# Kernel tuning notes

Hardware: AMD Instinct MI355X
Metric: run time of the kernel (lower is better)

## Reference

```python
import jax, jax.numpy as jnp
import numpy as np

EMBED_DIM = 1024
NUM_HEADS = 16
HEAD_DIM = EMBED_DIM // NUM_HEADS
HIDDEN_DIM = int(EMBED_DIM * 4.0)
LN_EPS = 1e-5


def layer_norm(x, g, b):
    mu = jnp.mean(x, axis=-1, keepdims=True)
    var = jnp.var(x, axis=-1, keepdims=True)
    return (x - mu) * jax.lax.rsqrt(var + LN_EPS) * g + b


def setup_inputs() -> dict:
    key = jax.random.key(0)
    ks = jax.random.split(key, 8)
    D, H3, Dh = EMBED_DIM, 3 * EMBED_DIM, HIDDEN_DIM
    s = lambda fan: 1.0 / np.sqrt(fan)
    return {
        "x": jax.random.normal(ks[0], (2, 2048, D), dtype=jnp.float32),
        "ln1_g": jnp.ones((D,), jnp.float32),
        "ln1_b": jnp.zeros((D,), jnp.float32),
        "ln2_g": jnp.ones((D,), jnp.float32),
        "ln2_b": jnp.zeros((D,), jnp.float32),
        "w_qkv": jax.random.normal(ks[1], (D, H3), jnp.float32) * s(D),
        "b_qkv": jnp.zeros((H3,), jnp.float32),
        "w_proj": jax.random.normal(ks[2], (D, D), jnp.float32) * s(D),
        "b_proj": jnp.zeros((D,), jnp.float32),
        "w_fc1": jax.random.normal(ks[3], (D, Dh), jnp.float32) * s(D),
        "b_fc1": jnp.zeros((Dh,), jnp.float32),
        "w_fc2": jax.random.normal(ks[4], (Dh, D), jnp.float32) * s(Dh),
        "b_fc2": jnp.zeros((D,), jnp.float32),
    }


def reference(x, ln1_g, ln1_b, ln2_g, ln2_b, w_qkv, b_qkv, w_proj, b_proj,
              w_fc1, b_fc1, w_fc2, b_fc2):
    B, N, D = x.shape
    H, hd = NUM_HEADS, HEAD_DIM

    # --- attention branch (dropout inactive at eval) ---
    h = layer_norm(x, ln1_g, ln1_b)
    qkv = h @ w_qkv + b_qkv                      # [B,N,3D]
    qkv = qkv.reshape(B, N, 3, H, hd)
    q = qkv[:, :, 0].transpose(0, 2, 1, 3)       # [B,H,N,hd]
    k = qkv[:, :, 1].transpose(0, 2, 1, 3)
    v = qkv[:, :, 2].transpose(0, 2, 1, 3)
    scores = jnp.einsum('bhqd,bhkd->bhqk', q, k) / jnp.sqrt(jnp.float32(hd))
    attn = jax.nn.softmax(scores, axis=-1)
    ctx = jnp.einsum('bhqk,bhkd->bhqd', attn, v) # [B,H,N,hd]
    ctx = ctx.transpose(0, 2, 1, 3).reshape(B, N, D)
    x = x + ctx @ w_proj + b_proj

    # --- MLP branch ---
    h2 = layer_norm(x, ln2_g, ln2_b)
    h2 = jax.nn.gelu(h2 @ w_fc1 + b_fc1, approximate=False)  # torch nn.GELU = exact erf
    x = x + h2 @ w_fc2 + b_fc2
    return x
```

## Files before the change

### kernel.cpp

```cpp
#include <hip/hip_runtime.h>
#include <hip/hip_bf16.h>
#include <cstdint>

typedef __attribute__((ext_vector_type(8))) short short8;
typedef __attribute__((ext_vector_type(4))) float f32x4;

__device__ __forceinline__ uint16_t f2b(float f) {
  uint32_t u = __builtin_bit_cast(uint32_t, f);
  return (uint16_t)((u + 0x7FFFu + ((u >> 16) & 1u)) >> 16);
}
__device__ __forceinline__ float b2f(uint16_t h) {
  uint32_t u = ((uint32_t)h) << 16;
  return __builtin_bit_cast(float, u);
}
__device__ __forceinline__ void async16(void* lds, const void* g) {
  __builtin_amdgcn_global_load_lds(
      (const __attribute__((address_space(1))) uint32_t*)g,
      (__attribute__((address_space(3))) uint32_t*)lds, 16, 0, 0);
}
__device__ __forceinline__ void xcd_remap(int& bx, int& by, int& bz) {
  int gx = gridDim.x, gy = gridDim.y;
  int nwg = gx * gy * gridDim.z;
  int hw = blockIdx.x + gx * (blockIdx.y + gy * blockIdx.z);
  int work = ((nwg & 7) == 0) ? ((hw & 7) * (nwg >> 3) + (hw >> 3)) : hw;
  bx = work % gx;
  int t = work / gx;
  by = t % gy;
  bz = t / gy;
}

__global__ __launch_bounds__(256) void k_transpose_all(
    const float* __restrict__ wq, const float* __restrict__ wp,
    const float* __restrict__ w1, const float* __restrict__ w2,
    uint16_t* __restrict__ tq, uint16_t* __restrict__ tp,
    uint16_t* __restrict__ t1, uint16_t* __restrict__ t2) {
  __shared__ float tile[64][65];
  int id = blockIdx.x;
  const float* w; uint16_t* wT; int K, N, bx, by;
  if (id < 768)        { w = wq; wT = tq; K = 1024; N = 3072; bx = id % 48; by = id / 48; }
  else if (id < 1024)  { id -= 768;  w = wp; wT = tp; K = 1024; N = 1024; bx = id & 15; by = id >> 4; }
  else if (id < 2048)  { id -= 1024; w = w1; wT = t1; K = 1024; N = 4096; bx = id & 63; by = id >> 6; }
  else                 { id -= 2048; w = w2; wT = t2; K = 4096; N = 1024; bx = id & 15; by = id >> 4; }
  const int tx = threadIdx.x;
  const int k0 = by * 64, n0 = bx * 64;
  const int cr = tx & 15, rbase = tx >> 4;
#pragma unroll
  for (int rr = 0; rr < 4; ++rr) {
    int k = rbase + rr * 16;
    int n = cr * 4;
    float4 v = *(const float4*)&w[(size_t)(k0 + k) * N + (n0 + n)];
    tile[k][n + 0] = v.x; tile[k][n + 1] = v.y;
    tile[k][n + 2] = v.z; tile[k][n + 3] = v.w;
  }
  __syncthreads();
#pragma unroll
  for (int rr = 0; rr < 4; ++rr) {
    int n = rbase + rr * 16;
    int k = cr * 4;
    ushort4 o;
    o.x = f2b(tile[k + 0][n]);
    o.y = f2b(tile[k + 1][n]);
    o.z = f2b(tile[k + 2][n]);
    o.w = f2b(tile[k + 3][n]);
    *(ushort4*)&wT[(size_t)(n0 + n) * K + (k0 + k)] = o;
  }
}

__global__ __launch_bounds__(256) void k_layernorm(
    const float* __restrict__ x, const float* __restrict__ g,
    const float* __restrict__ b, uint16_t* __restrict__ out) {
  const int row = blockIdx.x * 4 + (threadIdx.x >> 6);
  const int lane = threadIdx.x & 63;
  const float* xr = x + (size_t)row * 1024;
  float4 v[4];
  float s = 0.f, ss = 0.f;
#pragma unroll
  for (int i = 0; i < 4; ++i) {
    v[i] = *(const float4*)&xr[i * 256 + lane * 4];
    s += v[i].x + v[i].y + v[i].z + v[i].w;
    ss += v[i].x * v[i].x + v[i].y * v[i].y + v[i].z * v[i].z + v[i].w * v[i].w;
  }
#pragma unroll
  for (int off = 1; off < 64; off <<= 1) {
    s += __shfl_xor(s, off);
    ss += __shfl_xor(ss, off);
  }
  float mu = s * (1.f / 1024.f);
  float rstd = rsqrtf(ss * (1.f / 1024.f) - mu * mu + 1e-5f);
#pragma unroll
  for (int i = 0; i < 4; ++i) {
    int col = i * 256 + lane * 4;
    float4 gv = *(const float4*)&g[col];
    float4 bv = *(const float4*)&b[col];
    ushort4 o;
    o.x = f2b((v[i].x - mu) * rstd * gv.x + bv.x);
    o.y = f2b((v[i].y - mu) * rstd * gv.y + bv.y);
    o.z = f2b((v[i].z - mu) * rstd * gv.z + bv.z);
    o.w = f2b((v[i].w - mu) * rstd * gv.w + bv.w);
    *(ushort4*)&out[(size_t)row * 1024 + col] = o;
  }
}

__global__ __launch_bounds__(256) void k_ln2_fuse(
    const float* __restrict__ x, const uint16_t* __restrict__ pp0,
    const uint16_t* __restrict__ pp1, const float* __restrict__ bias,
    const float* __restrict__ g, const float* __restrict__ b,
    float* __restrict__ x2, uint16_t* __restrict__ out) {
  const int row = blockIdx.x * 4 + (threadIdx.x >> 6);
  const int lane = threadIdx.x & 63;
  const size_t rb = (size_t)row * 1024;
  float4 v[4];
  float s = 0.f, ss = 0.f;
#pragma unroll
  for (int i = 0; i < 4; ++i) {
    int col = i * 256 + lane * 4;
    float4 xv = *(const float4*)&x[rb + col];
    float4 bv = *(const float4*)&bias[col];
    ushort4 a0 = *(const ushort4*)&pp0[rb + col];
    ushort4 a1 = *(const ushort4*)&pp1[rb + col];
    v[i].x = xv.x + bv.x + b2f(a0.x) + b2f(a1.x);
    v[i].y = xv.y + bv.y + b2f(a0.y) + b2f(a1.y);
    v[i].z = xv.z + bv.z + b2f(a0.z) + b2f(a1.z);
    v[i].w = xv.w + bv.w + b2f(a0.w) + b2f(a1.w);
    *(float4*)&x2[rb + col] = v[i];
    s += v[i].x + v[i].y + v[i].z + v[i].w;
    ss += v[i].x * v[i].x + v[i].y * v[i].y + v[i].z * v[i].z + v[i].w * v[i].w;
  }
#pragma unroll
  for (int off = 1; off < 64; off <<= 1) {
    s += __shfl_xor(s, off);
    ss += __shfl_xor(ss, off);
  }
  float mu = s * (1.f / 1024.f);
  float rstd = rsqrtf(ss * (1.f / 1024.f) - mu * mu + 1e-5f);
#pragma unroll
  for (int i = 0; i < 4; ++i) {
    int col = i * 256 + lane * 4;
    float4 gv = *(const float4*)&g[col];
    float4 bv = *(const float4*)&b[col];
    ushort4 o;
    o.x = f2b((v[i].x - mu) * rstd * gv.x + bv.x);
    o.y = f2b((v[i].y - mu) * rstd * gv.y + bv.y);
    o.z = f2b((v[i].z - mu) * rstd * gv.z + bv.z);
    o.w = f2b((v[i].w - mu) * rstd * gv.w + bv.w);
    *(ushort4*)&out[rb + col] = o;
  }
}

__global__ __launch_bounds__(256) void k_fc2_reduce(
    const float* __restrict__ x2, const uint16_t* __restrict__ f0,
    const uint16_t* __restrict__ f1, const uint16_t* __restrict__ f2,
    const uint16_t* __restrict__ f3, const float* __restrict__ bias,
    float* __restrict__ out, int N) {
  int i = (blockIdx.x * 256 + threadIdx.x) * 4;
  float4 v = *(const float4*)&x2[i];
  float4 bv = *(const float4*)&bias[i & (N - 1)];
  ushort4 a0 = *(const ushort4*)&f0[i];
  ushort4 a1 = *(const ushort4*)&f1[i];
  ushort4 a2 = *(const ushort4*)&f2[i];
  ushort4 a3 = *(const ushort4*)&f3[i];
  v.x += bv.x + b2f(a0.x) + b2f(a1.x) + b2f(a2.x) + b2f(a3.x);
  v.y += bv.y + b2f(a0.y) + b2f(a1.y) + b2f(a2.y) + b2f(a3.y);
  v.z += bv.z + b2f(a0.z) + b2f(a1.z) + b2f(a2.z) + b2f(a3.z);
  v.w += bv.w + b2f(a0.w) + b2f(a1.w) + b2f(a2.w) + b2f(a3.w);
  *(float4*)&out[i] = v;
}

template <int EPI>
__global__ __launch_bounds__(256) void k_gemm(
    const uint16_t* __restrict__ A, const uint16_t* __restrict__ Bt,
    const float* __restrict__ bias, void* __restrict__ Cout,
    uint16_t* __restrict__ vTout, int M, int N, int K) {
  __shared__ __align__(16) uint16_t Alds[128 * 64];
  __shared__ __align__(16) uint16_t Blds[128 * 64];
  int bx, by, bz;
  xcd_remap(bx, by, bz);
  const int tid = threadIdx.x;
  const int lane = tid & 63;
  const int w = tid >> 6;
  const int wr = w >> 1, wc = w & 1;
  const int m0 = by * 128, n0 = bx * 128;
  const int l15 = lane & 15, l4 = lane >> 4;
  f32x4 acc[4][4] = {};
  for (int k0 = 0; k0 < K; k0 += 64) {
#pragma unroll
    for (int c = 0; c < 4; ++c) {
      int i = c * 256 + tid;
      int row = i >> 3, d = (i & 7) * 8;
      async16(&Alds[i * 8], &A[(size_t)(m0 + row) * K + k0 + d]);
    }
#pragma unroll
    for (int c = 0; c < 4; ++c) {
      int i = c * 256 + tid;
      int row = i >> 3, d = (i & 7) * 8;
      async16(&Blds[i * 8], &Bt[(size_t)(n0 + row) * K + k0 + d]);
    }
    __syncthreads();
#pragma unroll
    for (int kc = 0; kc < 2; ++kc) {
      short8 af[4], bf[4];
#pragma unroll
      for (int m = 0; m < 4; ++m)
        af[m] = *(const short8*)&Alds[(wr * 64 + m * 16 + l15) * 64 + kc * 32 + l4 * 8];
#pragma unroll
      for (int n = 0; n < 4; ++n)
        bf[n] = *(const short8*)&Blds[(wc * 64 + n * 16 + l15) * 64 + kc * 32 + l4 * 8];
#pragma unroll
      for (int m = 0; m < 4; ++m)
#pragma unroll
        for (int n = 0; n < 4; ++n)
          acc[m][n] = __builtin_amdgcn_mfma_f32_16x16x32_bf16(af[m], bf[n], acc[m][n], 0, 0, 0);
    }
    __syncthreads();
  }
#pragma unroll
  for (int m = 0; m < 4; ++m) {
#pragma unroll
    for (int n = 0; n < 4; ++n) {
      int col = n0 + wc * 64 + n * 16 + l15;
      int rowb = m0 + wr * 64 + m * 16 + l4 * 4;
      float bv = bias[col];
      if constexpr (EPI == 3) {
        if (col >= 2048) {
          int dtot = col - 2048;
          int hh = dtot >> 6, dd = dtot & 63;
          int bg = rowb >> 11, tl = rowb & 2047;
          ushort4 ov;
          ov.x = f2b(acc[m][n][0] + bv);
          ov.y = f2b(acc[m][n][1] + bv);
          ov.z = f2b(acc[m][n][2] + bv);
          ov.w = f2b(acc[m][n][3] + bv);
          *(ushort4*)&vTout[(((size_t)(bg * 16 + hh)) * 64 + dd) * 2048 + tl] = ov;
          continue;
        }
      }
#pragma unroll
      for (int r = 0; r < 4; ++r) {
        float val = acc[m][n][r] + bv;
        size_t idx = (size_t)(rowb + r) * N + col;
        if constexpr (EPI == 2) {
          float u = val * val;
          float a = fmaf(u, 0.1029480545f, 2.3022078158f);
          float t = exp2f(val * a);
          float gl = val - val / (t + 1.0f);
          ((uint16_t*)Cout)[idx] = f2b(gl);
        } else {
          ((uint16_t*)Cout)[idx] = f2b(val);
        }
      }
    }
  }
}

__global__ __launch_bounds__(256) void k_gemm_splitk(
    const uint16_t* __restrict__ A, const uint16_t* __restrict__ Bt,
    uint16_t* __restrict__ p0, uint16_t* __restrict__ p1,
    uint16_t* __restrict__ p2, uint16_t* __restrict__ p3,
    int M, int N, int K, int Kc) {
  __shared__ __align__(16) uint16_t Alds[128 * 64];
  __shared__ __align__(16) uint16_t Blds[128 * 64];
  int bx, by, bz;
  xcd_remap(bx, by, bz);
  const int tid = threadIdx.x;
  const int lane = tid & 63;
  const int w = tid >> 6;
  const int wr = w >> 1, wc = w & 1;
  const int m0 = by * 128, n0 = bx * 128;
  const int l15 = lane & 15, l4 = lane >> 4;
  const int kbeg = bz * Kc, kend = kbeg + Kc;
  uint16_t* __restrict__ P = (bz == 0) ? p0 : (bz == 1) ? p1 : (bz == 2) ? p2 : p3;
  f32x4 acc[4][4] = {};
  for (int k0 = kbeg; k0 < kend; k0 += 64) {
#pragma unroll
    for (int c = 0; c < 4; ++c) {
      int i = c * 256 + tid;
      int row = i >> 3, d = (i & 7) * 8;
      async16(&Alds[i * 8], &A[(size_t)(m0 + row) * K + k0 + d]);
    }
#pragma unroll
    for (int c = 0; c < 4; ++c) {
      int i = c * 256 + tid;
      int row = i >> 3, d = (i & 7) * 8;
      async16(&Blds[i * 8], &Bt[(size_t)(n0 + row) * K + k0 + d]);
    }
    __syncthreads();
#pragma unroll
    for (int kc = 0; kc < 2; ++kc) {
      short8 af[4], bf[4];
#pragma unroll
      for (int m = 0; m < 4; ++m)
        af[m] = *(const short8*)&Alds[(wr * 64 + m * 16 + l15) * 64 + kc * 32 + l4 * 8];
#pragma unroll
      for (int n = 0; n < 4; ++n)
        bf[n] = *(const short8*)&Blds[(wc * 64 + n * 16 + l15) * 64 + kc * 32 + l4 * 8];
#pragma unroll
      for (int m = 0; m < 4; ++m)
#pragma unroll
        for (int n = 0; n < 4; ++n)
          acc[m][n] = __builtin_amdgcn_mfma_f32_16x16x32_bf16(af[m], bf[n], acc[m][n], 0, 0, 0);
    }
    __syncthreads();
  }
#pragma unroll
  for (int m = 0; m < 4; ++m) {
#pragma unroll
    for (int n = 0; n < 4; ++n) {
      int col = n0 + wc * 64 + n * 16 + l15;
      int rowb = m0 + wr * 64 + m * 16 + l4 * 4;
#pragma unroll
      for (int r = 0; r < 4; ++r)
        P[(size_t)(rowb + r) * N + col] = f2b(acc[m][n][r]);
    }
  }
}

__global__ __launch_bounds__(256) void k_attn(
    const uint16_t* __restrict__ qkv, const uint16_t* __restrict__ vT,
    uint16_t* __restrict__ ctx) {
  __shared__ __align__(16) uint16_t Klds[2][64 * 64];
  __shared__ __align__(16) uint16_t Vlds[2][64 * 64];
  __shared__ __align__(16) uint16_t Plds[4][32 * 64];
  __shared__ __align__(16) float bc[4][2][16];
  int bx, by, bz;
  xcd_remap(bx, by, bz);
  const int bh = by, qt = bx;
  const int b = bh >> 4, h = bh & 15;
  const int tid = threadIdx.x, lane = tid & 63, w = tid >> 6;
  const int l15 = lane & 15, l4 = lane >> 4;
  const int sw = (l15 & 7) << 3;
  const size_t tokbase = (size_t)b * 2048;

  const float QSC = 0.125f * 1.44269504088896340736f;
  short8 qa[2][2];
#pragma unroll
  for (int g = 0; g < 2; ++g) {
    const int qrow = qt * 128 + w * 32 + g * 16 + l15;
#pragma unroll
    for (int kc = 0; kc < 2; ++kc) {
      short8 v = *(const short8*)&qkv[(tokbase + qrow) * 3072 + h * 64 + kc * 32 + l4 * 8];
#pragma unroll
      for (int j = 0; j < 8; ++j) v[j] = (short)f2b(b2f((uint16_t)v[j]) * QSC);
      qa[g][kc] = v;
    }
  }
  short8 ones;
#pragma unroll
  for (int j = 0; j < 8; ++j) ones[j] = (short)0x3F80;

  float m_s[2] = {-1e30f, -1e30f};
  f32x4 o[2][4] = {};
  f32x4 ol[2] = {};

  auto stage = [&](int buf, int t0) {
#pragma unroll
    for (int c = 0; c < 2; ++c) {
      int i = c * 256 + tid;
      int row = i >> 3, colE = (i & 7) * 8;
      int colS = colE ^ ((row & 7) << 3);
      async16(&Klds[buf][i * 8],
              &qkv[(tokbase + t0 + row) * 3072 + 1024 + h * 64 + colS]);
    }
#pragma unroll
    for (int c = 0; c < 2; ++c) {
      int i = c * 256 + tid;
      int row = i >> 3, tkE = (i & 7) * 8;
      int tkS = tkE ^ ((row & 7) << 3);
      async16(&Vlds[buf][i * 8],
              &vT[((size_t)bh * 64 + row) * 2048 + t0 + tkS]);
    }
  };

  stage(0, 0);
  __syncthreads();
  int cur = 0;

  for (int t0 = 0; t0 < 2048; t0 += 64) {
    if (t0 + 64 < 2048) stage(cur ^ 1, t0 + 64);

    f32x4 s[2][4] = {};
    __builtin_amdgcn_s_setprio(1);
#pragma unroll
    for (int kc = 0; kc < 2; ++kc) {
      const int cc = (kc * 32 + l4 * 8) ^ sw;
#pragma unroll
      for (int c = 0; c < 4; ++c) {
        short8 kf = *(const short8*)&Klds[cur][(c * 16 + l15) * 64 + cc];
        s[0][c] = __builtin_amdgcn_mfma_f32_16x16x32_bf16(kf, qa[0][kc], s[0][c], 0, 0, 0);
        s[1][c] = __builtin_amdgcn_mfma_f32_16x16x32_bf16(kf, qa[1][kc], s[1][c], 0, 0, 0);
      }
    }
    __builtin_amdgcn_s_setprio(0);

#pragma unroll
    for (int g = 0; g < 2; ++g) {
      float a0 = fmaxf(fmaxf(s[g][0][0], s[g][0][1]), fmaxf(s[g][0][2], s[g][0][3]));
      float a1 = fmaxf(fmaxf(s[g][1][0], s[g][1][1]), fmaxf(s[g][1][2], s[g][1][3]));
      float a2 = fmaxf(fmaxf(s[g][2][0], s[g][2][1]), fmaxf(s[g][2][2], s[g][2][3]));
      float a3 = fmaxf(fmaxf(s[g][3][0], s[g][3][1]), fmaxf(s[g][3][2], s[g][3][3]));
      float pml = fmaxf(fmaxf(a0, a1), fmaxf(a2, a3));
      if (!__all(pml - m_s[g] <= 8.f)) {
        float pm = pml;
        pm = fmaxf(pm, __shfl_xor(pm, 16));
        pm = fmaxf(pm, __shfl_xor(pm, 32));
        float mn = fmaxf(m_s[g], pm);
        float scale = exp2f(m_s[g] - mn);
        m_s[g] = mn;
        if (lane < 16) bc[w][g][lane] = scale;
        f32x4 sc = *(const f32x4*)&bc[w][g][l4 * 4];
#pragma unroll
        for (int df = 0; df < 4; ++df)
#pragma unroll
          for (int r = 0; r < 4; ++r) o[g][df][r] *= sc[r];
#pragma unroll
        for (int r = 0; r < 4; ++r) ol[g][r] *= sc[r];
      }
#pragma unroll
      for (int c = 0; c < 4; ++c) {
        float p0 = exp2f(s[g][c][0] - m_s[g]);
        float p1 = exp2f(s[g][c][1] - m_s[g]);
        float p2 = exp2f(s[g][c][2] - m_s[g]);
        float p3 = exp2f(s[g][c][3] - m_s[g]);
        uint32_t lo, hi;
        asm("v_cvt_pk_bf16_f32 %0, %1, %2" : "=v"(lo) : "v"(p0), "v"(p1));
        asm("v_cvt_pk_bf16_f32 %0, %1, %2" : "=v"(hi) : "v"(p2), "v"(p3));
        *(uint2*)&Plds[w][(g * 16 + l15) * 64 + ((c * 16 + l4 * 4) ^ sw)] =
            make_uint2(lo, hi);
      }
    }

    __builtin_amdgcn_s_setprio(1);
#pragma unroll
    for (int kc = 0; kc < 2; ++kc) {
      const int cc = (kc * 32 + l4 * 8) ^ sw;
      short8 pa0 = *(const short8*)&Plds[w][l15 * 64 + cc];
      short8 pa1 = *(const short8*)&Plds[w][(16 + l15) * 64 + cc];
      ol[0] = __builtin_amdgcn_mfma_f32_16x16x32_bf16(pa0, ones, ol[0], 0, 0, 0);
      ol[1] = __builtin_amdgcn_mfma_f32_16x16x32_bf16(pa1, ones, ol[1], 0, 0, 0);
#pragma unroll
      for (int df = 0; df < 4; ++df) {
        short8 vf = *(const short8*)&Vlds[cur][(df * 16 + l15) * 64 + cc];
        o[0][df] = __builtin_amdgcn_mfma_f32_16x16x32_bf16(pa0, vf, o[0][df], 0, 0, 0);
        o[1][df] = __builtin_amdgcn_mfma_f32_16x16x32_bf16(pa1, vf, o[1][df], 0, 0, 0);
      }
    }
    __builtin_amdgcn_s_setprio(0);
    __syncthreads();
    cur ^= 1;
  }

#pragma unroll
  for (int g = 0; g < 2; ++g) {
#pragma unroll
    for (int r = 0; r < 4; ++r) {
      float rl = 1.0f / ol[g][r];
      int tok = qt * 128 + w * 32 + g * 16 + l4 * 4 + r;
#pragma unroll
      for (int df = 0; df < 4; ++df) {
        ctx[(tokbase + tok) * 1024 + h * 64 + df * 16 + l15] = f2b(o[g][df][r] * rl);
      }
    }
  }
}

extern "C" void kernel_launch(void* const* d_in, const int* in_sizes, int n_in,
                              void* d_out, int out_size, void* d_ws, size_t ws_size,
                              hipStream_t stream) {
  const float* x      = (const float*)d_in[0];
  const float* ln1_g  = (const float*)d_in[1];
  const float* ln1_b  = (const float*)d_in[2];
  const float* ln2_g  = (const float*)d_in[3];
  const float* ln2_b  = (const float*)d_in[4];
  const float* w_qkv  = (const float*)d_in[5];
  const float* b_qkv  = (const float*)d_in[6];
  const float* w_proj = (const float*)d_in[7];
  const float* b_proj = (const float*)d_in[8];
  const float* w_fc1  = (const float*)d_in[9];
  const float* b_fc1  = (const float*)d_in[10];
  const float* w_fc2  = (const float*)d_in[11];
  const float* b_fc2  = (const float*)d_in[12];
  float* out = (float*)d_out;
  char* ws = (char*)d_ws;
  const size_t MB = 1 << 20;

  uint16_t* wTfc1  = (uint16_t*)(ws + 0 * MB);
  uint16_t* wTfc2  = (uint16_t*)(ws + 8 * MB);
  uint16_t* wTqkv  = (uint16_t*)(ws + 16 * MB);
  uint16_t* wTproj = (uint16_t*)(ws + 22 * MB);
  uint16_t* hbuf   = (uint16_t*)(ws + 24 * MB);
  uint16_t* qkvb   = (uint16_t*)(ws + 32 * MB);
  uint16_t* vTb    = (uint16_t*)(ws + 56 * MB);
  uint16_t* ctxb   = (uint16_t*)(ws + 64 * MB);
  float*    x2b    = (float*)   (ws + 72 * MB);
  uint16_t* pp0    = (uint16_t*)(ws + 32 * MB);
  uint16_t* pp1    = (uint16_t*)(ws + 40 * MB);
  uint16_t* actb   = (uint16_t*)(ws + 32 * MB);
  uint16_t* fp0    = (uint16_t*)(ws + 16 * MB);
  uint16_t* fp1    = (uint16_t*)(ws + 24 * MB);
  uint16_t* fp2    = (uint16_t*)(ws + 64 * MB);
  uint16_t* fp3    = (uint16_t*)(ws + 0 * MB);

  k_transpose_all<<<3072, 256, 0, stream>>>(w_qkv, w_proj, w_fc1, w_fc2,
                                            wTqkv, wTproj, wTfc1, wTfc2);

  k_layernorm<<<1024, 256, 0, stream>>>(x, ln1_g, ln1_b, hbuf);
  k_gemm<3><<<dim3(24, 32), 256, 0, stream>>>(hbuf, wTqkv, b_qkv, qkvb, vTb, 4096, 3072, 1024);
  k_attn<<<dim3(16, 32), 256, 0, stream>>>(qkvb, vTb, ctxb);

  k_gemm_splitk<<<dim3(8, 32, 2), 256, 0, stream>>>(ctxb, wTproj, pp0, pp1, pp0, pp0,
                                                    4096, 1024, 1024, 512);
  k_ln2_fuse<<<1024, 256, 0, stream>>>(x, pp0, pp1, b_proj, ln2_g, ln2_b, x2b, hbuf);

  k_gemm<2><<<dim3(32, 32), 256, 0, stream>>>(hbuf, wTfc1, b_fc1, actb, nullptr, 4096, 4096, 1024);

  k_gemm_splitk<<<dim3(8, 32, 4), 256, 0, stream>>>(actb, wTfc2, fp0, fp1, fp2, fp3,
                                                    4096, 1024, 4096, 1024);
  k_fc2_reduce<<<4096, 256, 0, stream>>>(x2b, fp0, fp1, fp2, fp3, b_fc2, out, 1024);
}
```

Measured before the change: 310.1 us.

## Load K/V fragments directly from global memory in attention, halve query tile

The attention kernel no longer stages K and V tiles in double-buffered LDS with async loads and block barriers. Each wave now reads its K and V MFMA fragments straight from global memory (relying on cache reuse across waves), and handles 16 query rows instead of 32. The grid doubles to 1024 blocks, and the launch bound asks for 4 blocks per CU. The softmax rescale broadcast moves from LDS to shuffles. This drops the __syncthreads and LDS staging cost, but adds redundant global/L2 traffic, since every wave reloads the same K/V, and halves K/V reuse per fragment load.

Measured after the change: 460.1 us. 1.48x slower.

```diff
diff --git a/kernel.cpp b/kernel.cpp
--- a/kernel.cpp
+++ b/kernel.cpp
@@ -314,13 +314,10 @@
   }
 }
 
-__global__ __launch_bounds__(256) void k_attn(
+__global__ __launch_bounds__(256, 4) void k_attn(
     const uint16_t* __restrict__ qkv, const uint16_t* __restrict__ vT,
     uint16_t* __restrict__ ctx) {
-  __shared__ __align__(16) uint16_t Klds[2][64 * 64];
-  __shared__ __align__(16) uint16_t Vlds[2][64 * 64];
-  __shared__ __align__(16) uint16_t Plds[4][32 * 64];
-  __shared__ __align__(16) float bc[4][2][16];
+  __shared__ __align__(16) uint16_t Plds[4][16 * 64];
   int bx, by, bz;
   xcd_remap(bx, by, bz);
   const int bh = by, qt = bx;
@@ -331,133 +328,103 @@
   const size_t tokbase = (size_t)b * 2048;
 
   const float QSC = 0.125f * 1.44269504088896340736f;
-  short8 qa[2][2];
-#pragma unroll
-  for (int g = 0; g < 2; ++g) {
-    const int qrow = qt * 128 + w * 32 + g * 16 + l15;
+  short8 qa[2];
+  const int qrow = qt * 64 + w * 16 + l15;
+#pragma unroll
+  for (int kc = 0; kc < 2; ++kc) {
+    short8 v = *(const short8*)&qkv[(tokbase + qrow) * 3072 + h * 64 + kc * 32 + l4 * 8];
+#pragma unroll
+    for (int j = 0; j < 8; ++j) v[j] = (short)f2b(b2f((uint16_t)v[j]) * QSC);
+    qa[kc] = v;
+  }
+  short8 ones;
+#pragma unroll
+  for (int j = 0; j < 8; ++j) ones[j] = (short)0x3F80;
+
+  float m_s = -1e30f;
+  f32x4 o[4] = {};
+  f32x4 ol = {};
+
+  const uint16_t* Kbase = qkv + tokbase * 3072 + 1024 + h * 64;
+  const uint16_t* Vbase = vT + (size_t)bh * 64 * 2048;
+
+  for (int t0 = 0; t0 < 2048; t0 += 64) {
+    f32x4 s[4] = {};
 #pragma unroll
     for (int kc = 0; kc < 2; ++kc) {
-      short8 v = *(const short8*)&qkv[(tokbase + qrow) * 3072 + h * 64 + kc * 32 + l4 * 8];
-#pragma unroll
-      for (int j = 0; j < 8; ++j) v[j] = (short)f2b(b2f((uint16_t)v[j]) * QSC);
-      qa[g][kc] = v;
-    }
-  }
-  short8 ones;
-#pragma unroll
-  for (int j = 0; j < 8; ++j) ones[j] = (short)0x3F80;
-
-  float m_s[2] = {-1e30f, -1e30f};
-  f32x4 o[2][4] = {};
-  f32x4 ol[2] = {};
-
-  auto stage = [&](int buf, int t0) {
-#pragma unroll
-    for (int c = 0; c < 2; ++c) {
-      int i = c * 256 + tid;
-      int row = i >> 3, colE = (i & 7) * 8;
-      int colS = colE ^ ((row & 7) << 3);
-      async16(&Klds[buf][i * 8],
-              &qkv[(tokbase + t0 + row) * 3072 + 1024 + h * 64 + colS]);
-    }
-#pragma unroll
-    for (int c = 0; c < 2; ++c) {
-      int i = c * 256 + tid;
-      int row = i >> 3, tkE = (i & 7) * 8;
-      int tkS = tkE ^ ((row & 7) << 3);
-      async16(&Vlds[buf][i * 8],
-              &vT[((size_t)bh * 64 + row) * 2048 + t0 + tkS]);
-    }
-  };
-
-  stage(0, 0);
-  __syncthreads();
-  int cur = 0;
-
-  for (int t0 = 0; t0 < 2048; t0 += 64) {
-    if (t0 + 64 < 2048) stage(cur ^ 1, t0 + 64);
-
-    f32x4 s[2][4] = {};
-    __builtin_amdgcn_s_setprio(1);
-#pragma unroll
-    for (int kc = 0; kc < 2; ++kc) {
-      const int cc = (kc * 32 + l4 * 8) ^ sw;
-#pragma unroll
-      for (int c = 0; c < 4; ++c) {
-        short8 kf = *(const short8*)&Klds[cur][(c * 16 + l15) * 64 + cc];
-        s[0][c] = __builtin_amdgcn_mfma_f32_16x16x32_bf16(kf, qa[0][kc], s[0][c], 0, 0, 0);
-        s[1][c] = __builtin_amdgcn_mfma_f32_16x16x32_bf16(kf, qa[1][kc], s[1][c], 0, 0, 0);
-      }
-    }
-    __builtin_amdgcn_s_setprio(0);
-
-#pragma unroll
-    for (int g = 0; g < 2; ++g) {
-      float a0 = fmaxf(fmaxf(s[g][0][0], s[g][0][1]), fmaxf(s[g][0][2], s[g][0][3]));
-      float a1 = fmaxf(fmaxf(s[g][1][0], s[g][1][1]), fmaxf(s[g][1][2], s[g][1][3]));
-      float a2 = fmaxf(fmaxf(s[g][2][0], s[g][2][1]), fmaxf(s[g][2][2], s[g][2][3]));
-      float a3 = fmaxf(fmaxf(s[g][3][0], s[g][3][1]), fmaxf(s[g][3][2], s[g][3][3]));
+      short8 kf[4];
+#pragma unroll
+      for (int c = 0; c < 4; ++c)
+        kf[c] = *(const short8*)&Kbase[(size_t)(t0 + c * 16 + l15) * 3072 + kc * 32 + l4 * 8];
+      __builtin_amdgcn_s_setprio(1);
+#pragma unroll
+      for (int c = 0; c < 4; ++c)
+        s[c] = __builtin_amdgcn_mfma_f32_16x16x32_bf16(kf[c], qa[kc], s[c], 0, 0, 0);
+      __builtin_amdgcn_s_setprio(0);
+    }
+
+    short8 vf[2][4];
+#pragma unroll
+    for (int kc = 0; kc < 2; ++kc)
+#pragma unroll
+      for (int df = 0; df < 4; ++df)
+        vf[kc][df] = *(const short8*)&Vbase[(size_t)(df * 16 + l15) * 2048 + t0 + kc * 32 + l4 * 8];
+
+    {
+      float a0 = fmaxf(fmaxf(s[0][0], s[0][1]), fmaxf(s[0][2], s[0][3]));
+      float a1 = fmaxf(fmaxf(s[1][0], s[1][1]), fmaxf(s[1][2], s[1][3]));
+      float a2 = fmaxf(fmaxf(s[2][0], s[2][1]), fmaxf(s[2][2], s[2][3]));
+      float a3 = fmaxf(fmaxf(s[3][0], s[3][1]), fmaxf(s[3][2], s[3][3]));
       float pml = fmaxf(fmaxf(a0, a1), fmaxf(a2, a3));
-      if (!__all(pml - m_s[g] <= 8.f)) {
+      if (!__all(pml - m_s <= 8.f)) {
         float pm = pml;
         pm = fmaxf(pm, __shfl_xor(pm, 16));
         pm = fmaxf(pm, __shfl_xor(pm, 32));
-        float mn = fmaxf(m_s[g], pm);
-        float scale = exp2f(m_s[g] - mn);
-        m_s[g] = mn;
-        if (lane < 16) bc[w][g][lane] = scale;
-        f32x4 sc = *(const f32x4*)&bc[w][g][l4 * 4];
-#pragma unroll
-        for (int df = 0; df < 4; ++df)
-#pragma unroll
-          for (int r = 0; r < 4; ++r) o[g][df][r] *= sc[r];
-#pragma unroll
-        for (int r = 0; r < 4; ++r) ol[g][r] *= sc[r];
+        float mn = fmaxf(m_s, pm);
+        float scale = exp2f(m_s - mn);
+        m_s = mn;
+        float sc0 = __shfl(scale, l4 * 4 + 0);
+        float sc1 = __shfl(scale, l4 * 4 + 1);
+        float sc2 = __shfl(scale, l4 * 4 + 2);
+        float sc3 = __shfl(scale, l4 * 4 + 3);
+#pragma unroll
+        for (int df = 0; df < 4; ++df) {
+          o[df][0] *= sc0; o[df][1] *= sc1; o[df][2] *= sc2; o[df][3] *= sc3;
+        }
+        ol[0] *= sc0; ol[1] *= sc1; ol[2] *= sc2; ol[3] *= sc3;
       }
 #pragma unroll
       for (int c = 0; c < 4; ++c) {
-        float p0 = exp2f(s[g][c][0] - m_s[g]);
-        float p1 = exp2f(s[g][c][1] - m_s[g]);
-        float p2 = exp2f(s[g][c][2] - m_s[g]);
-        float p3 = exp2f(s[g][c][3] - m_s[g]);
+        float p0 = exp2f(s[c][0] - m_s);
+        float p1 = exp2f(s[c][1] - m_s);
+        float p2 = exp2f(s[c][2] - m_s);
+        float p3 = exp2f(s[c][3] - m_s);
         uint32_t lo, hi;
         asm("v_cvt_pk_bf16_f32 %0, %1, %2" : "=v"(lo) : "v"(p0), "v"(p1));
         asm("v_cvt_pk_bf16_f32 %0, %1, %2" : "=v"(hi) : "v"(p2), "v"(p3));
-        *(uint2*)&Plds[w][(g * 16 + l15) * 64 + ((c * 16 + l4 * 4) ^ sw)] =
-            make_uint2(lo, hi);
+        *(uint2*)&Plds[w][l15 * 64 + ((c * 16 + l4 * 4) ^ sw)] = make_uint2(lo, hi);
       }
     }
 
     __builtin_amdgcn_s_setprio(1);
 #pragma unroll
     for (int kc = 0; kc < 2; ++kc) {
-      const int cc = (kc * 32 + l4 * 8) ^ sw;
-      short8 pa0 = *(const short8*)&Plds[w][l15 * 64 + cc];
-      short8 pa1 = *(const short8*)&Plds[w][(16 + l15) * 64 + cc];
-      ol[0] = __builtin_amdgcn_mfma_f32_16x16x32_bf16(pa0, ones, ol[0], 0, 0, 0);
-      ol[1] = __builtin_amdgcn_mfma_f32_16x16x32_bf16(pa1, ones, ol[1], 0, 0, 0);
-#pragma unroll
-      for (int df = 0; df < 4; ++df) {
-        short8 vf = *(const short8*)&Vlds[cur][(df * 16 + l15) * 64 + cc];
-        o[0][df] = __builtin_amdgcn_mfma_f32_16x16x32_bf16(pa0, vf, o[0][df], 0, 0, 0);
-        o[1][df] = __builtin_amdgcn_mfma_f32_16x16x32_bf16(pa1, vf, o[1][df], 0, 0, 0);
-      }
+      short8 pa = *(const short8*)&Plds[w][l15 * 64 + ((kc * 32 + l4 * 8) ^ sw)];
+      ol = __builtin_amdgcn_mfma_f32_16x16x32_bf16(pa, ones, ol, 0, 0, 0);
+#pragma unroll
+      for (int df = 0; df < 4; ++df)
+        o[df] = __builtin_amdgcn_mfma_f32_16x16x32_bf16(pa, vf[kc][df], o[df], 0, 0, 0);
     }
     __builtin_amdgcn_s_setprio(0);
-    __syncthreads();
-    cur ^= 1;
-  }
-
-#pragma unroll
-  for (int g = 0; g < 2; ++g) {
-#pragma unroll
-    for (int r = 0; r < 4; ++r) {
-      float rl = 1.0f / ol[g][r];
-      int tok = qt * 128 + w * 32 + g * 16 + l4 * 4 + r;
-#pragma unroll
-      for (int df = 0; df < 4; ++df) {
-        ctx[(tokbase + tok) * 1024 + h * 64 + df * 16 + l15] = f2b(o[g][df][r] * rl);
-      }
+  }
+
+#pragma unroll
+  for (int r = 0; r < 4; ++r) {
+    float rl = 1.0f / ol[r];
+    int tok = qt * 64 + w * 16 + l4 * 4 + r;
+#pragma unroll
+    for (int df = 0; df < 4; ++df) {
+      ctx[(tokbase + tok) * 1024 + h * 64 + df * 16 + l15] = f2b(o[df][r] * rl);
     }
   }
 }
@@ -504,7 +471,7 @@
 
   k_layernorm<<<1024, 256, 0, stream>>>(x, ln1_g, ln1_b, hbuf);
   k_gemm<3><<<dim3(24, 32), 256, 0, stream>>>(hbuf, wTqkv, b_qkv, qkvb, vTb, 4096, 3072, 1024);
-  k_attn<<<dim3(16, 32), 256, 0, stream>>>(qkvb, vTb, ctxb);
+  k_attn<<<dim3(32, 32), 256, 0, stream>>>(qkvb, vTb, ctxb);
 
   k_gemm_splitk<<<dim3(8, 32, 2), 256, 0, stream>>>(ctxb, wTproj, pp0, pp1, pp0, pp0,
                                                     4096, 1024, 1024, 512);
```
